# Kernel optimization log

Hardware: AMD Instinct MI355X
Metric: run time of the kernel (lower is better)

The kernel has to match this reference:

```python
import jax, jax.numpy as jnp
import numpy as np

B, S, D, H = 512, 200, 512, 8
DH = D // H
LN_EPS = 1e-12


def layer_norm(x, g, b):
    mu = jnp.mean(x, axis=-1, keepdims=True)
    var = jnp.var(x, axis=-1, keepdims=True)
    return (x - mu) / jnp.sqrt(var + LN_EPS) * g + b


def setup_inputs() -> dict:
    key = jax.random.key(0)
    ks = jax.random.split(key, 8)
    s = 0.02
    return {
        "input_tensor": jax.random.normal(ks[0], (B, S, D), jnp.float32),
        "position_embedding": jax.random.normal(ks[1], (B, S, D), jnp.float32),
        "attention_mask": jnp.ones((B, 1, S), jnp.int32),
        "Wq": jax.random.normal(ks[2], (D, D), jnp.float32) * s,
        "bq": jnp.zeros((D,), jnp.float32),
        "Wk": jax.random.normal(ks[3], (D, D), jnp.float32) * s,
        "bk": jnp.zeros((D,), jnp.float32),
        "Wv": jax.random.normal(ks[4], (D, D), jnp.float32) * s,
        "bv": jnp.zeros((D,), jnp.float32),
        "Wd": jax.random.normal(ks[5], (D, D), jnp.float32) * s,
        "bd": jnp.zeros((D,), jnp.float32),
        "ln_g": jnp.ones((D,), jnp.float32),
        "ln_b": jnp.zeros((D,), jnp.float32),
    }


def reference(input_tensor, position_embedding, attention_mask,
              Wq, bq, Wk, bk, Wv, bv, Wd, bd, ln_g, ln_b):
    # sequence_input = input + positional embedding (Multifaceted_Attention_Mixer.forward)
    x = input_tensor + position_embedding
    # LinMHA: pre-LayerNorm (dropout is identity at eval); attention_mask is unused by LinMHA
    h = layer_norm(x, ln_g, ln_b)
    # QKV projections, split into heads: [B, H, S, DH]
    q = (h @ Wq + bq).reshape(B, S, H, DH).transpose(0, 2, 1, 3)
    k = (h @ Wk + bk).reshape(B, S, H, DH).transpose(0, 2, 1, 3)
    v = (h @ Wv + bv).reshape(B, S, H, DH).transpose(0, 2, 1, 3)
    # ELU feature maps + per-token L2 normalization over the head dim
    eq = jax.nn.elu(q)
    ek = jax.nn.elu(k)  # torch permutes K to [B,H,DH,S] and L2-norms over dim=2 (=DH) -> same as per-row norm here
    qn = eq / jnp.linalg.norm(eq, axis=-1, keepdims=True)
    kn = ek / jnp.linalg.norm(ek, axis=-1, keepdims=True)
    # linear attention: Q (K^T V) instead of softmax(QK^T)V
    kv = jnp.einsum('bhsd,bhse->bhde', kn, v)          # [B,H,DH,DH]
    ctx = jnp.einsum('bhsd,bhde->bhse', qn, kv) / np.float32(np.sqrt(DH))
    ctx = ctx.transpose(0, 2, 1, 3).reshape(B, S, D)
    out = ctx @ Wd + bd
    # residual with the LayerNormed input (LinMHA reassigns input_tensor = LayerNorm(input))
    out = layer_norm(out + h, ln_g, ln_b)
    # Mixer: output = reshape(x, [B, 200, H*d_k])
    return out.reshape(B, 200, D)
```

## Files before the change

### kernel.cpp

```cpp
#include <hip/hip_runtime.h>

typedef __bf16 bf16_t;
typedef __attribute__((ext_vector_type(8))) __bf16 bf16x8;
typedef __attribute__((ext_vector_type(4))) float f32x4;

#define DMODEL 512
#define SEQ 200
#define NHEAD 8
#define DH 64
#define BTOT 512
#define QKVW 1536

__device__ __forceinline__ float wave_sum(float v) {
#pragma unroll
    for (int m = 32; m >= 1; m >>= 1) v += __shfl_xor(v, m);
    return v;
}

__device__ __forceinline__ void load8f(const void* p, size_t off, int f32, float x[8]) {
    if (f32) {
        const f32x4* q = (const f32x4*)((const float*)p + off);
        f32x4 a = q[0], b = q[1];
#pragma unroll
        for (int j = 0; j < 4; ++j) { x[j] = a[j]; x[4 + j] = b[j]; }
    } else {
        bf16x8 u = *(const bf16x8*)((const bf16_t*)p + off);
#pragma unroll
        for (int j = 0; j < 8; ++j) x[j] = (float)u[j];
    }
}
__device__ __forceinline__ void store8f(void* p, size_t off, int f32, const float x[8]) {
    if (f32) {
        f32x4 a, b;
#pragma unroll
        for (int j = 0; j < 4; ++j) { a[j] = x[j]; b[j] = x[4 + j]; }
        f32x4* q = (f32x4*)((float*)p + off);
        q[0] = a; q[1] = b;
    } else {
        bf16x8 u;
#pragma unroll
        for (int j = 0; j < 8; ++j) u[j] = (__bf16)x[j];
        *(bf16x8*)((bf16_t*)p + off) = u;
    }
}
__device__ __forceinline__ float load1f(const void* p, size_t off, int f32) {
    return f32 ? ((const float*)p)[off] : (float)((const bf16_t*)p)[off];
}

__device__ __forceinline__ void gload16(const bf16_t* g, bf16_t* l) {
    __builtin_amdgcn_global_load_lds(
        (const __attribute__((address_space(1))) void*)g,
        (__attribute__((address_space(3))) void*)l,
        16, 0, 0);
}

__global__ __launch_bounds__(256)
void probe_dtype(const void* p, int* flag)
{
    const bf16_t* b = (const bf16_t*)p;
    int tid = threadIdx.x;
    float mx = 0.f;
    for (int i = tid; i < 65536; i += 256) {
        float v = fabsf((float)b[i]);
        if (!(v == v)) v = 1e30f;
        mx = fmaxf(mx, v);
    }
#pragma unroll
    for (int m = 32; m >= 1; m >>= 1) mx = fmaxf(mx, __shfl_xor(mx, m));
    __shared__ float wmax[4];
    int wave = tid >> 6, lane = tid & 63;
    if (lane == 0) wmax[wave] = mx;
    __syncthreads();
    if (tid == 0) {
        float m2 = fmaxf(fmaxf(wmax[0], wmax[1]), fmaxf(wmax[2], wmax[3]));
        *flag = (m2 > 1e3f) ? 1 : 0;
    }
}

__global__ __launch_bounds__(256)
void transpose_w(const void* w0, const void* w1, const void* w2, const void* w3,
                 bf16_t* __restrict__ wt, const int* flagp)
{
    int f32 = *flagp;
    __shared__ bf16_t tile[32][33];
    const void* srcs[4] = {w0, w1, w2, w3};
    const void* src = srcs[blockIdx.z];
    bf16_t* dst = wt + (size_t)blockIdx.z * DMODEL * DMODEL;
    int tx = threadIdx.x, ty = threadIdx.y;
    int bx = blockIdx.x * 32, by = blockIdx.y * 32;
#pragma unroll
    for (int i = 0; i < 32; i += 8)
        tile[ty + i][tx] = (__bf16)load1f(src, (size_t)(by + ty + i) * DMODEL + bx + tx, f32);
    __syncthreads();
#pragma unroll
    for (int i = 0; i < 32; i += 8)
        dst[(size_t)(bx + ty + i) * DMODEL + by + tx] = tile[tx][ty + i];
}

__global__ __launch_bounds__(256)
void addln_in(const void* a, const void* c, const void* g, const void* beta,
              bf16_t* __restrict__ out, size_t base, const int* flagp)
{
    int f32 = *flagp;
    int wave = threadIdx.x >> 6, lane = threadIdx.x & 63;
    size_t row = (size_t)blockIdx.x * 4 + wave;
    size_t off = base + row * DMODEL + (size_t)lane * 8;
    float xa[8], xc[8];
    load8f(a, off, f32, xa);
    load8f(c, off, f32, xc);
    float x[8]; float s = 0.f, ss = 0.f;
#pragma unroll
    for (int j = 0; j < 8; ++j) {
        x[j] = xa[j] + xc[j];
        s += x[j]; ss += x[j] * x[j];
    }
    s = wave_sum(s); ss = wave_sum(ss);
    float mu = s * (1.f / DMODEL);
    float var = ss * (1.f / DMODEL) - mu * mu;
    float rstd = rsqrtf(var + 1e-12f);
    float vg[8], vb[8];
    load8f(g,    (size_t)lane * 8, f32, vg);
    load8f(beta, (size_t)lane * 8, f32, vb);
    bf16x8 o;
#pragma unroll
    for (int j = 0; j < 8; ++j)
        o[j] = (__bf16)((x[j] - mu) * rstd * vg[j] + vb[j]);
    *(bf16x8*)(out + row * DMODEL + (size_t)lane * 8) = o;
}

__global__ __launch_bounds__(256)
void addln_out(const bf16_t* __restrict__ a, int lda, const bf16_t* __restrict__ c, int ldc2,
               const void* g, const void* beta, void* out, size_t obase,
               const int* flagp)
{
    int f32 = *flagp;
    int wave = threadIdx.x >> 6, lane = threadIdx.x & 63;
    size_t row = (size_t)blockIdx.x * 4 + wave;
    bf16x8 va = *(const bf16x8*)(a + row * (size_t)lda  + (size_t)lane * 8);
    bf16x8 vc = *(const bf16x8*)(c + row * (size_t)ldc2 + (size_t)lane * 8);
    float x[8]; float s = 0.f, ss = 0.f;
#pragma unroll
    for (int j = 0; j < 8; ++j) {
        x[j] = (float)va[j] + (float)vc[j];
        s += x[j]; ss += x[j] * x[j];
    }
    s = wave_sum(s); ss = wave_sum(ss);
    float mu = s * (1.f / DMODEL);
    float var = ss * (1.f / DMODEL) - mu * mu;
    float rstd = rsqrtf(var + 1e-12f);
    float vg[8], vb[8];
    load8f(g,    (size_t)lane * 8, f32, vg);
    load8f(beta, (size_t)lane * 8, f32, vb);
    float o[8];
#pragma unroll
    for (int j = 0; j < 8; ++j)
        o[j] = (x[j] - mu) * rstd * vg[j] + vb[j];
    store8f(out, obase + row * DMODEL + (size_t)lane * 8, f32, o);
}

__global__ __launch_bounds__(256)
void gemm_fused(const bf16_t* A, int lda,
                const bf16_t* __restrict__ BT,
                const void* b0, const void* b1, const void* b2,
                bf16_t* C, int ldc,
                int K, int elun, const int* flagp)
{
    int f32 = *flagp;
    __shared__ alignas(16) bf16_t As[128][32];
    __shared__ alignas(16) bf16_t Bs[128][32];
    int tid = threadIdx.x;
    int wave = tid >> 6, lane = tid & 63, lm = lane & 15, quad = lane >> 4;
    int m0 = blockIdx.y * 128, n0 = blockIdx.x * 128;
    int wm = (wave >> 1) * 64, wn = (wave & 1) * 64;
    int r0 = tid >> 2, c0 = (tid & 3) * 8;

    const bf16_t* ga = A  + (size_t)(m0 + r0) * lda + c0;
    const bf16_t* gb = BT + (size_t)(n0 + r0) * K   + c0;
    bf16_t* lasa = &As[0][0] + wave * 512;
    bf16_t* lasb = &Bs[0][0] + wave * 512;

    f32x4 zero = {0.f, 0.f, 0.f, 0.f};
    f32x4 acc[4][4];
#pragma unroll
    for (int i = 0; i < 4; ++i)
#pragma unroll
        for (int j = 0; j < 4; ++j) acc[i][j] = zero;

    for (int k0 = 0; k0 < K; k0 += 32) {
        __syncthreads();
        gload16(ga + k0,                      lasa);
        gload16(ga + k0 + (size_t)64 * lda,   lasa + 2048);
        gload16(gb + k0,                      lasb);
        gload16(gb + k0 + (size_t)64 * K,     lasb + 2048);
        __syncthreads();
        bf16x8 af[4], bfr[4];
#pragma unroll
        for (int i = 0; i < 4; ++i) af[i]  = *(const bf16x8*)&As[wm + i * 16 + lm][quad * 8];
#pragma unroll
        for (int j = 0; j < 4; ++j) bfr[j] = *(const bf16x8*)&Bs[wn + j * 16 + lm][quad * 8];
#pragma unroll
        for (int i = 0; i < 4; ++i)
#pragma unroll
            for (int j = 0; j < 4; ++j)
                acc[i][j] = __builtin_amdgcn_mfma_f32_16x16x32_bf16(af[i], bfr[j], acc[i][j], 0, 0, 0);
    }

    const void* bp = b0;
    if (elun) { if (n0 >= 1024) bp = b2; else if (n0 >= 512) bp = b1; }
    float bvv[4];
#pragma unroll
    for (int j = 0; j < 4; ++j)
        bvv[j] = load1f(bp, (size_t)((n0 + wn + j * 16 + lm) & (DMODEL - 1)), f32);
#pragma unroll
    for (int i = 0; i < 4; ++i)
#pragma unroll
        for (int j = 0; j < 4; ++j)
#pragma unroll
            for (int r = 0; r < 4; ++r) acc[i][j][r] += bvv[j];

    if (elun && n0 < 1024) {
#pragma unroll
        for (int i = 0; i < 4; ++i)
#pragma unroll
            for (int r = 0; r < 4; ++r) {
                float e[4]; float ss = 0.f;
#pragma unroll
                for (int j = 0; j < 4; ++j) {
                    float v = acc[i][j][r];
                    float t = v > 0.f ? v : expm1f(v);
                    e[j] = t; ss += t * t;
                }
                ss += __shfl_xor(ss, 1); ss += __shfl_xor(ss, 2);
                ss += __shfl_xor(ss, 4); ss += __shfl_xor(ss, 8);
                float rs = rsqrtf(ss);
#pragma unroll
                for (int j = 0; j < 4; ++j) acc[i][j][r] = e[j] * rs;
            }
    }
#pragma unroll
    for (int j = 0; j < 4; ++j) {
        int col = n0 + wn + j * 16 + lm;
#pragma unroll
        for (int i = 0; i < 4; ++i)
#pragma unroll
            for (int r = 0; r < 4; ++r) {
                int row = m0 + wm + i * 16 + quad * 4 + r;
                C[(size_t)row * ldc + col] = (__bf16)acc[i][j][r];
            }
    }
}

__global__ __launch_bounds__(256)
void kvctx_kernel(bf16_t* qkv)
{
    __shared__ alignas(16) bf16_t knT[64][232];
    __shared__ alignas(16) bf16_t vT [64][232];
    int bh = blockIdx.x; int b = bh >> 3, h = bh & 7;
    int tid = threadIdx.x;
    size_t base = (size_t)b * SEQ * QKVW + (size_t)h * DH;
    const bf16_t* kp = qkv + base + 512;
    const bf16_t* vp = qkv + base + 1024;
    for (int idx = tid; idx < SEQ * DH; idx += 256) {
        int s = idx >> 6, d = idx & 63;
        knT[d][s] = kp[(size_t)s * QKVW + d];
        vT [d][s] = vp[(size_t)s * QKVW + d];
    }
    for (int idx = tid; idx < 64 * 32; idx += 256) {
        int d = idx >> 5, s = SEQ + (idx & 31);
        knT[d][s] = (__bf16)0.f;
        vT [d][s] = (__bf16)0.f;
    }
    __syncthreads();
    int wave = tid >> 6, lane = tid & 63, lm = lane & 15, quad = lane >> 4;
    int dbase = wave * 16;
    f32x4 zero = {0.f, 0.f, 0.f, 0.f};
    f32x4 acc[4];
#pragma unroll
    for (int in = 0; in < 4; ++in) acc[in] = zero;
#pragma unroll
    for (int k0 = 0; k0 < 224; k0 += 32) {
        bf16x8 a = *(const bf16x8*)&knT[dbase + lm][k0 + quad * 8];
#pragma unroll
        for (int in = 0; in < 4; ++in) {
            bf16x8 bb = *(const bf16x8*)&vT[in * 16 + lm][k0 + quad * 8];
            acc[in] = __builtin_amdgcn_mfma_f32_16x16x32_bf16(a, bb, acc[in], 0, 0, 0);
        }
    }
    __syncthreads();
    bf16_t* kvs = &knT[0][0];
#pragma unroll
    for (int in = 0; in < 4; ++in)
#pragma unroll
        for (int r = 0; r < 4; ++r)
            kvs[(size_t)(in * 16 + lm) * 72 + dbase + quad * 4 + r] = (__bf16)acc[in][r];
    __syncthreads();
    bf16x8 bfr[2][4];
#pragma unroll
    for (int ks = 0; ks < 2; ++ks)
#pragma unroll
        for (int in = 0; in < 4; ++in)
            bfr[ks][in] = *(const bf16x8*)&kvs[(size_t)(in * 16 + lm) * 72 + ks * 32 + quad * 8];
    bf16_t* qp = qkv + base;
    for (int mt = wave; mt < 13; mt += 4) {
        int m0 = mt * 16;
        int sA = m0 + lm; if (sA > SEQ - 1) sA = SEQ - 1;
        f32x4 a2[4];
#pragma unroll
        for (int in = 0; in < 4; ++in) a2[in] = zero;
#pragma unroll
        for (int ks = 0; ks < 2; ++ks) {
            bf16x8 a = *(const bf16x8*)&qp[(size_t)sA * QKVW + ks * 32 + quad * 8];
#pragma unroll
            for (int in = 0; in < 4; ++in)
                a2[in] = __builtin_amdgcn_mfma_f32_16x16x32_bf16(a, bfr[ks][in], a2[in], 0, 0, 0);
        }
#pragma unroll
        for (int in = 0; in < 4; ++in)
#pragma unroll
            for (int r = 0; r < 4; ++r) {
                int s = m0 + quad * 4 + r;
                if (s < SEQ)
                    qp[(size_t)s * QKVW + in * 16 + lm] = (__bf16)(a2[in][r] * 0.125f);
            }
    }
}

extern "C" void kernel_launch(void* const* d_in, const int* in_sizes, int n_in,
                              void* d_out, int out_size, void* d_ws, size_t ws_size,
                              hipStream_t stream)
{
    const void* input = d_in[0];
    const void* pos   = d_in[1];
    const void* Wq = d_in[3];
    const void* bq = d_in[4];
    const void* Wk = d_in[5];
    const void* bk = d_in[6];
    const void* Wv = d_in[7];
    const void* bv = d_in[8];
    const void* Wd = d_in[9];
    const void* bd = d_in[10];
    const void* g  = d_in[11];
    const void* be = d_in[12];

    int chunkb = 64;
    {
        size_t base_need = 256 + (size_t)4 * DMODEL * DMODEL * 2;
        size_t per_b = (size_t)SEQ * (DMODEL + QKVW) * 2;
        if (ws_size >= base_need + (size_t)128 * per_b) chunkb = 128;
    }
    int nchunk = BTOT / chunkb;
    int crows = chunkb * SEQ;

    int* flag   = (int*)d_ws;
    bf16_t* WT  = (bf16_t*)((char*)d_ws + 256);
    bf16_t* h_c = WT  + (size_t)4 * DMODEL * DMODEL;
    bf16_t* qkv = h_c + (size_t)crows * DMODEL;

    probe_dtype<<<dim3(1), 256, 0, stream>>>(input, flag);
    transpose_w<<<dim3(16, 16, 4), dim3(32, 8), 0, stream>>>(Wq, Wk, Wv, Wd, WT, flag);

    for (int c = 0; c < nchunk; ++c) {
        size_t roff = (size_t)c * crows * DMODEL;
        addln_in<<<dim3(crows / 4), 256, 0, stream>>>(input, pos, g, be, h_c, roff, flag);
        gemm_fused<<<dim3(QKVW / 128, crows / 128), 256, 0, stream>>>(
            h_c, DMODEL, WT, bq, bk, bv, qkv, QKVW, DMODEL, 1, flag);
        kvctx_kernel<<<dim3(chunkb * NHEAD), 256, 0, stream>>>(qkv);
        gemm_fused<<<dim3(DMODEL / 128, crows / 128), 256, 0, stream>>>(
            qkv, QKVW, WT + (size_t)3 * DMODEL * DMODEL, bd, bd, bd,
            qkv + 1024, QKVW, DMODEL, 0, flag);
        addln_out<<<dim3(crows / 4), 256, 0, stream>>>(
            qkv + 1024, QKVW, h_c, DMODEL, g, be, d_out, roff, flag);
    }
}
```

Measured before the change: 1.231 ms.

## Widen GEMM K-tile with swizzled LDS, fuse residual, merge LN kernels across chunks

The GEMM K-step grows from 32 to 64, with XOR-swizzled LDS columns to avoid bank conflicts and a workgroup remap for L2 locality. Weight rows are permuted so each lane owns four contiguous output columns, which allows vectorized bf16x4 stores and fuses the residual add into the output-projection epilogue. The output LayerNorm of chunk c and the input LayerNorm of chunk c+1 now run in one launch, cutting the launch count and the separate residual read. The risks are more LDS per block, which may lower occupancy, and correctness that depends on the permuted weight layout matching the epilogue indexing.

```diff
diff --git a/kernel.cpp b/kernel.cpp
--- a/kernel.cpp
+++ b/kernel.cpp
@@ -2,6 +2,7 @@
 
 typedef __bf16 bf16_t;
 typedef __attribute__((ext_vector_type(8))) __bf16 bf16x8;
+typedef __attribute__((ext_vector_type(4))) __bf16 bf16x4;
 typedef __attribute__((ext_vector_type(4))) float f32x4;
 
 #define DMODEL 512
@@ -52,6 +53,10 @@
         (const __attribute__((address_space(1))) void*)g,
         (__attribute__((address_space(3))) void*)l,
         16, 0, 0);
+}
+
+__device__ __forceinline__ int permrow(int n) {
+    return (n & ~63) | ((n & 3) * 16) | ((n & 63) >> 2);
 }
 
 __global__ __launch_bounds__(256)
@@ -94,90 +99,85 @@
     __syncthreads();
 #pragma unroll
     for (int i = 0; i < 32; i += 8)
-        dst[(size_t)(bx + ty + i) * DMODEL + by + tx] = tile[tx][ty + i];
-}
-
-__global__ __launch_bounds__(256)
-void addln_in(const void* a, const void* c, const void* g, const void* beta,
-              bf16_t* __restrict__ out, size_t base, const int* flagp)
+        dst[(size_t)permrow(bx + ty + i) * DMODEL + by + tx] = tile[tx][ty + i];
+}
+
+__global__ __launch_bounds__(256)
+void addln_dual(const bf16_t* __restrict__ aprev, const void* g, const void* beta,
+                void* out, size_t obase,
+                const void* in, const void* pos, bf16_t* __restrict__ hout, size_t ibase,
+                int nout, const int* flagp)
 {
     int f32 = *flagp;
     int wave = threadIdx.x >> 6, lane = threadIdx.x & 63;
-    size_t row = (size_t)blockIdx.x * 4 + wave;
-    size_t off = base + row * DMODEL + (size_t)lane * 8;
-    float xa[8], xc[8];
-    load8f(a, off, f32, xa);
-    load8f(c, off, f32, xc);
+    int bid = blockIdx.x;
     float x[8]; float s = 0.f, ss = 0.f;
-#pragma unroll
-    for (int j = 0; j < 8; ++j) {
-        x[j] = xa[j] + xc[j];
-        s += x[j]; ss += x[j] * x[j];
-    }
-    s = wave_sum(s); ss = wave_sum(ss);
-    float mu = s * (1.f / DMODEL);
-    float var = ss * (1.f / DMODEL) - mu * mu;
-    float rstd = rsqrtf(var + 1e-12f);
-    float vg[8], vb[8];
-    load8f(g,    (size_t)lane * 8, f32, vg);
-    load8f(beta, (size_t)lane * 8, f32, vb);
-    bf16x8 o;
-#pragma unroll
-    for (int j = 0; j < 8; ++j)
-        o[j] = (__bf16)((x[j] - mu) * rstd * vg[j] + vb[j]);
-    *(bf16x8*)(out + row * DMODEL + (size_t)lane * 8) = o;
-}
-
-__global__ __launch_bounds__(256)
-void addln_out(const bf16_t* __restrict__ a, int lda, const bf16_t* __restrict__ c, int ldc2,
-               const void* g, const void* beta, void* out, size_t obase,
-               const int* flagp)
-{
-    int f32 = *flagp;
-    int wave = threadIdx.x >> 6, lane = threadIdx.x & 63;
-    size_t row = (size_t)blockIdx.x * 4 + wave;
-    bf16x8 va = *(const bf16x8*)(a + row * (size_t)lda  + (size_t)lane * 8);
-    bf16x8 vc = *(const bf16x8*)(c + row * (size_t)ldc2 + (size_t)lane * 8);
-    float x[8]; float s = 0.f, ss = 0.f;
-#pragma unroll
-    for (int j = 0; j < 8; ++j) {
-        x[j] = (float)va[j] + (float)vc[j];
-        s += x[j]; ss += x[j] * x[j];
-    }
-    s = wave_sum(s); ss = wave_sum(ss);
-    float mu = s * (1.f / DMODEL);
-    float var = ss * (1.f / DMODEL) - mu * mu;
-    float rstd = rsqrtf(var + 1e-12f);
-    float vg[8], vb[8];
-    load8f(g,    (size_t)lane * 8, f32, vg);
-    load8f(beta, (size_t)lane * 8, f32, vb);
-    float o[8];
-#pragma unroll
-    for (int j = 0; j < 8; ++j)
-        o[j] = (x[j] - mu) * rstd * vg[j] + vb[j];
-    store8f(out, obase + row * DMODEL + (size_t)lane * 8, f32, o);
+    if (bid < nout) {
+        size_t row = (size_t)bid * 4 + wave;
+        bf16x8 va = *(const bf16x8*)(aprev + row * QKVW + (size_t)lane * 8);
+#pragma unroll
+        for (int j = 0; j < 8; ++j) { x[j] = (float)va[j]; s += x[j]; ss += x[j] * x[j]; }
+        s = wave_sum(s); ss = wave_sum(ss);
+        float mu = s * (1.f / DMODEL);
+        float rstd = rsqrtf(ss * (1.f / DMODEL) - mu * mu + 1e-12f);
+        float vg[8], vb[8];
+        load8f(g,    (size_t)lane * 8, f32, vg);
+        load8f(beta, (size_t)lane * 8, f32, vb);
+        float o[8];
+#pragma unroll
+        for (int j = 0; j < 8; ++j) o[j] = (x[j] - mu) * rstd * vg[j] + vb[j];
+        store8f(out, obase + row * DMODEL + (size_t)lane * 8, f32, o);
+    } else {
+        size_t row = (size_t)(bid - nout) * 4 + wave;
+        size_t off = ibase + row * DMODEL + (size_t)lane * 8;
+        float xa[8], xc[8];
+        load8f(in,  off, f32, xa);
+        load8f(pos, off, f32, xc);
+#pragma unroll
+        for (int j = 0; j < 8; ++j) { x[j] = xa[j] + xc[j]; s += x[j]; ss += x[j] * x[j]; }
+        s = wave_sum(s); ss = wave_sum(ss);
+        float mu = s * (1.f / DMODEL);
+        float rstd = rsqrtf(ss * (1.f / DMODEL) - mu * mu + 1e-12f);
+        float vg[8], vb[8];
+        load8f(g,    (size_t)lane * 8, f32, vg);
+        load8f(beta, (size_t)lane * 8, f32, vb);
+        bf16x8 o;
+#pragma unroll
+        for (int j = 0; j < 8; ++j)
+            o[j] = (__bf16)((x[j] - mu) * rstd * vg[j] + vb[j]);
+        *(bf16x8*)(hout + row * DMODEL + (size_t)lane * 8) = o;
+    }
 }
 
 __global__ __launch_bounds__(256)
 void gemm_fused(const bf16_t* A, int lda,
                 const bf16_t* __restrict__ BT,
                 const void* b0, const void* b1, const void* b2,
+                const bf16_t* __restrict__ resid, int ldr,
                 bf16_t* C, int ldc,
                 int K, int elun, const int* flagp)
 {
     int f32 = *flagp;
-    __shared__ alignas(16) bf16_t As[128][32];
-    __shared__ alignas(16) bf16_t Bs[128][32];
+    __shared__ alignas(16) bf16_t As[128][64];
+    __shared__ alignas(16) bf16_t Bs[128][64];
     int tid = threadIdx.x;
     int wave = tid >> 6, lane = tid & 63, lm = lane & 15, quad = lane >> 4;
-    int m0 = blockIdx.y * 128, n0 = blockIdx.x * 128;
+
+    int gx = gridDim.x;
+    int nwg = gx * gridDim.y;
+    int lin = blockIdx.y * gx + blockIdx.x;
+    int nl = lin;
+    if ((nwg & 7) == 0) nl = (lin & 7) * (nwg >> 3) + (lin >> 3);
+    int m0 = (nl / gx) * 128, n0 = (nl % gx) * 128;
+
     int wm = (wave >> 1) * 64, wn = (wave & 1) * 64;
-    int r0 = tid >> 2, c0 = (tid & 3) * 8;
-
-    const bf16_t* ga = A  + (size_t)(m0 + r0) * lda + c0;
-    const bf16_t* gb = BT + (size_t)(n0 + r0) * K   + c0;
-    bf16_t* lasa = &As[0][0] + wave * 512;
-    bf16_t* lasb = &Bs[0][0] + wave * 512;
+
+    int row_l = lane >> 3;
+    int colsw = ((lane & 7) * 8) ^ (row_l * 8);
+    const bf16_t* gaw = A  + (size_t)(m0 + wave * 8 + row_l) * lda + colsw;
+    const bf16_t* gbw = BT + (size_t)(n0 + wave * 8 + row_l) * K   + colsw;
+    bf16_t* la = &As[0][0] + wave * 512;
+    bf16_t* lb = &Bs[0][0] + wave * 512;
 
     f32x4 zero = {0.f, 0.f, 0.f, 0.f};
     f32x4 acc[4][4];
@@ -186,31 +186,38 @@
 #pragma unroll
         for (int j = 0; j < 4; ++j) acc[i][j] = zero;
 
-    for (int k0 = 0; k0 < K; k0 += 32) {
+    int xsw = (lm & 7) * 8;
+    for (int k0 = 0; k0 < K; k0 += 64) {
         __syncthreads();
-        gload16(ga + k0,                      lasa);
-        gload16(ga + k0 + (size_t)64 * lda,   lasa + 2048);
-        gload16(gb + k0,                      lasb);
-        gload16(gb + k0 + (size_t)64 * K,     lasb + 2048);
+#pragma unroll
+        for (int q = 0; q < 4; ++q) {
+            gload16(gaw + k0 + (size_t)(q * 32) * lda, la + q * 2048);
+            gload16(gbw + k0 + (size_t)(q * 32) * K,   lb + q * 2048);
+        }
         __syncthreads();
-        bf16x8 af[4], bfr[4];
-#pragma unroll
-        for (int i = 0; i < 4; ++i) af[i]  = *(const bf16x8*)&As[wm + i * 16 + lm][quad * 8];
-#pragma unroll
-        for (int j = 0; j < 4; ++j) bfr[j] = *(const bf16x8*)&Bs[wn + j * 16 + lm][quad * 8];
-#pragma unroll
-        for (int i = 0; i < 4; ++i)
-#pragma unroll
-            for (int j = 0; j < 4; ++j)
-                acc[i][j] = __builtin_amdgcn_mfma_f32_16x16x32_bf16(af[i], bfr[j], acc[i][j], 0, 0, 0);
+#pragma unroll
+        for (int kk = 0; kk < 2; ++kk) {
+            int x = (kk * 32 + quad * 8) ^ xsw;
+            bf16x8 af[4], bfr[4];
+#pragma unroll
+            for (int i = 0; i < 4; ++i) af[i]  = *(const bf16x8*)&As[wm + i * 16 + lm][x];
+#pragma unroll
+            for (int j = 0; j < 4; ++j) bfr[j] = *(const bf16x8*)&Bs[wn + j * 16 + lm][x];
+#pragma unroll
+            for (int i = 0; i < 4; ++i)
+#pragma unroll
+                for (int j = 0; j < 4; ++j)
+                    acc[i][j] = __builtin_amdgcn_mfma_f32_16x16x32_bf16(af[i], bfr[j], acc[i][j], 0, 0, 0);
+        }
     }
 
     const void* bp = b0;
     if (elun) { if (n0 >= 1024) bp = b2; else if (n0 >= 512) bp = b1; }
+    int cb = n0 + wn + 4 * lm;
     float bvv[4];
 #pragma unroll
     for (int j = 0; j < 4; ++j)
-        bvv[j] = load1f(bp, (size_t)((n0 + wn + j * 16 + lm) & (DMODEL - 1)), f32);
+        bvv[j] = load1f(bp, (size_t)((cb + j) & (DMODEL - 1)), f32);
 #pragma unroll
     for (int i = 0; i < 4; ++i)
 #pragma unroll
@@ -238,16 +245,24 @@
             }
     }
 #pragma unroll
-    for (int j = 0; j < 4; ++j) {
-        int col = n0 + wn + j * 16 + lm;
-#pragma unroll
-        for (int i = 0; i < 4; ++i)
-#pragma unroll
-            for (int r = 0; r < 4; ++r) {
-                int row = m0 + wm + i * 16 + quad * 4 + r;
-                C[(size_t)row * ldc + col] = (__bf16)acc[i][j][r];
+    for (int i = 0; i < 4; ++i)
+#pragma unroll
+        for (int r = 0; r < 4; ++r) {
+            int row = m0 + wm + i * 16 + quad * 4 + r;
+            float o[4];
+            if (resid) {
+                bf16x4 hv = *(const bf16x4*)&resid[(size_t)row * ldr + cb];
+#pragma unroll
+                for (int j = 0; j < 4; ++j) o[j] = acc[i][j][r] + (float)hv[j];
+            } else {
+#pragma unroll
+                for (int j = 0; j < 4; ++j) o[j] = acc[i][j][r];
             }
-    }
+            bf16x4 ov;
+#pragma unroll
+            for (int j = 0; j < 4; ++j) ov[j] = (__bf16)o[j];
+            *(bf16x4*)&C[(size_t)row * ldc + cb] = ov;
+        }
 }
 
 __global__ __launch_bounds__(256)
@@ -359,16 +374,21 @@
     probe_dtype<<<dim3(1), 256, 0, stream>>>(input, flag);
     transpose_w<<<dim3(16, 16, 4), dim3(32, 8), 0, stream>>>(Wq, Wk, Wv, Wd, WT, flag);
 
+    addln_dual<<<dim3(crows / 4), 256, 0, stream>>>(
+        (const bf16_t*)qkv, g, be, d_out, 0, input, pos, h_c, 0, 0, flag);
+
     for (int c = 0; c < nchunk; ++c) {
         size_t roff = (size_t)c * crows * DMODEL;
-        addln_in<<<dim3(crows / 4), 256, 0, stream>>>(input, pos, g, be, h_c, roff, flag);
         gemm_fused<<<dim3(QKVW / 128, crows / 128), 256, 0, stream>>>(
-            h_c, DMODEL, WT, bq, bk, bv, qkv, QKVW, DMODEL, 1, flag);
+            h_c, DMODEL, WT, bq, bk, bv, nullptr, 0, qkv, QKVW, DMODEL, 1, flag);
         kvctx_kernel<<<dim3(chunkb * NHEAD), 256, 0, stream>>>(qkv);
         gemm_fused<<<dim3(DMODEL / 128, crows / 128), 256, 0, stream>>>(
             qkv, QKVW, WT + (size_t)3 * DMODEL * DMODEL, bd, bd, bd,
-            qkv + 1024, QKVW, DMODEL, 0, flag);
-        addln_out<<<dim3(crows / 4), 256, 0, stream>>>(
-            qkv + 1024, QKVW, h_c, DMODEL, g, be, d_out, roff, flag);
-    }
-}
+            h_c, DMODEL, qkv + 1024, QKVW, DMODEL, 0, flag);
+        int nout = crows / 4;
+        int nin = (c + 1 < nchunk) ? crows / 4 : 0;
+        size_t ibase = (size_t)(c + 1) * crows * DMODEL;
+        addln_dual<<<dim3(nout + nin), 256, 0, stream>>>(
+            qkv + 1024, g, be, d_out, roff, input, pos, h_c, ibase, nout, flag);
+    }
+}
```

After: 1.166 ms. 1.06x faster.
